# Kernel optimization log

Measured on AMD Instinct MI355X. Metric: run time of the kernel, lower is better.

The kernel has to match this reference:

```python
import jax, jax.numpy as jnp
import numpy as np

N = 1024    # num_points
HID = 1024  # Hamiltonian MLP hidden width


def setup_inputs() -> dict:
    key = jax.random.key(0)
    ks = jax.random.split(key, 6)
    def w(k, shape, fan_in):
        return jax.random.normal(k, shape, dtype=jnp.float32) / np.float32(np.sqrt(fan_in))
    return {
        "x": jax.random.normal(ks[0], (N,), dtype=jnp.float32),
        "q": jax.random.normal(ks[1], (N,), dtype=jnp.float32),
        "p": jax.random.normal(ks[2], (N,), dtype=jnp.float32),
        "W1": w(ks[3], (3 * N, HID), 3 * N),
        "b1": jnp.zeros((HID,), dtype=jnp.float32),
        "W2": w(ks[4], (HID, HID), HID),
        "b2": jnp.zeros((HID,), dtype=jnp.float32),
        "W3": w(ks[5], (HID, 1), HID),
        "b3": jnp.zeros((1,), dtype=jnp.float32),
    }


def _hamiltonian(z, W1, b1, W2, b2, W3, b3):
    # H: R^{3N} -> scalar (matches self.H(cat([x,q,p])).sum())
    h = jnp.tanh(z @ W1 + b1)
    h = jnp.tanh(h @ W2 + b2)
    return jnp.sum(h @ W3 + b3)


def reference(x, q, p, W1, b1, W2, b2, W3, b3):
    n = x.shape[0]

    def grads_qp(x_):
        # (dH/dq, dH/dp) as a function of x, with q,p closed over
        f = lambda q_, p_: _hamiltonian(jnp.concatenate([x_, q_, p_]), W1, b1, W2, b2, W3, b3)
        return jax.grad(f, argnums=(0, 1))(q, p)  # each [n]

    # Diagonal of cross-Hessian blocks via forward-over-reverse, batched over
    # all n basis directions at once (replaces the per-index autograd loop).
    eye = jnp.eye(n, dtype=x.dtype)

    def diag_entry(e_i, i):
        _, (dgq, dgp) = jax.jvp(grads_qp, (x,), (e_i,))
        return dgq[i], dgp[i]  # d2H/(dx_i dq_i), d2H/(dx_i dp_i)

    dH_dq_dx, dH_dp_dx = jax.vmap(diag_entry)(eye, jnp.arange(n))  # each [n]
    return dH_dp_dx, -dH_dq_dx
```

## Files before the change

### kernel.cpp

```cpp
#include <hip/hip_runtime.h>
#include <math.h>

typedef unsigned short u16;
typedef __bf16 bf16x8 __attribute__((ext_vector_type(8)));
typedef float f32x4 __attribute__((ext_vector_type(4)));

__device__ inline u16 bf16_rn(float x) {
    unsigned u = __float_as_uint(x);
    return (u16)((u + 0x7FFFu + ((u >> 16) & 1u)) >> 16);
}
__device__ inline uint2 pack4(u16 a, u16 b, u16 c, u16 d) {
    uint2 r;
    r.x = (unsigned)a | ((unsigned)b << 16);
    r.y = (unsigned)c | ((unsigned)d << 16);
    return r;
}
__device__ inline uint2 pack4f(float a, float b, float c, float d) {
    return pack4(bf16_rn(a), bf16_rn(b), bf16_rn(c), bf16_rn(d));
}
__device__ inline f32x4 mfma16(bf16x8 a, bf16x8 b, f32x4 c) {
    return __builtin_amdgcn_mfma_f32_16x16x32_bf16(a, b, c, 0, 0, 0);
}

__global__ __launch_bounds__(256) void k_pre(const float* __restrict__ x,
                                             const float* __restrict__ q,
                                             const float* __restrict__ p,
                                             const float* __restrict__ W1,
                                             u16* __restrict__ Ah,
                                             float* __restrict__ Upart,
                                             float* __restrict__ out,
                                             float* __restrict__ Vacc) {
    int b = blockIdx.x, t = threadIdx.x;
    if (b < 192) {
        int jc = b;
        int k = (jc & 3) * 256 + t;
        int j0 = (jc >> 2) * 64;
        __shared__ float zs[64];
        if (t < 64) {
            int j = j0 + t;
            zs[t] = (j < 1024) ? x[j] : (j < 2048 ? q[j - 1024] : p[j - 2048]);
        }
        __syncthreads();
        float acc = 0.f;
        if (j0 < 1024) {
#pragma unroll 8
            for (int j = 0; j < 64; ++j) {
                float v = W1[(j0 + j) * 1024 + k];
                Ah[(j0 + j) * 1024 + k] = bf16_rn(v);
                acc += zs[j] * v;
            }
        } else {
#pragma unroll 8
            for (int j = 0; j < 64; ++j) acc += zs[j] * W1[(j0 + j) * 1024 + k];
        }
        Upart[(jc >> 2) * 1024 + k] = acc;
    } else {
        int idx = ((b - 192) * 256 + t) * 4;
        if (idx < 2048) *(float4*)(out + idx) = make_float4(0.f, 0.f, 0.f, 0.f);
        else *(float4*)(Vacc + idx - 2048) = make_float4(0.f, 0.f, 0.f, 0.f);
    }
}

__global__ __launch_bounds__(256) void k_w2v(const float* __restrict__ W2,
                                             const float* __restrict__ b1,
                                             const float* __restrict__ Upart,
                                             float* __restrict__ H1g, float* __restrict__ D1g,
                                             u16* __restrict__ W2h,
                                             u16* __restrict__ WTh,
                                             float* __restrict__ Vacc) {
    __shared__ float T[64][65];
    __shared__ float hs[64], ds[64];
    __shared__ float red[4][64];
    int k0 = blockIdx.y * 64, m0 = blockIdx.x * 64;
    int t = threadIdx.x;
    {
        int lk = t & 63, g = t >> 6;
        float u = 0.f;
#pragma unroll
        for (int c = 0; c < 12; ++c) u += Upart[(g * 12 + c) * 1024 + k0 + lk];
        red[g][lk] = u;
    }
    __syncthreads();
    if (t < 64) {
        float u = red[0][t] + red[1][t] + red[2][t] + red[3][t];
        float h = tanhf(u + b1[k0 + t]);
        hs[t] = h;
        ds[t] = 1.f - h * h;
        if (m0 == 0) { H1g[k0 + t] = h; D1g[k0 + t] = 1.f - h * h; }
    }
    __syncthreads();
    int rr = t >> 4, cc = (t & 15) * 4;
    float4 vp = make_float4(0.f, 0.f, 0.f, 0.f);
#pragma unroll
    for (int j = 0; j < 4; ++j) {
        int r = rr + j * 16;
        float4 v = *(const float4*)(W2 + (k0 + r) * 1024 + m0 + cc);
        T[r][cc + 0] = v.x; T[r][cc + 1] = v.y; T[r][cc + 2] = v.z; T[r][cc + 3] = v.w;
        *(uint2*)&W2h[(k0 + r) * 1024 + m0 + cc] = pack4f(v.x, v.y, v.z, v.w);
        float hk = hs[r];
        vp.x += hk * v.x; vp.y += hk * v.y; vp.z += hk * v.z; vp.w += hk * v.w;
    }
    vp.x += __shfl_xor(vp.x, 16); vp.y += __shfl_xor(vp.y, 16);
    vp.z += __shfl_xor(vp.z, 16); vp.w += __shfl_xor(vp.w, 16);
    vp.x += __shfl_xor(vp.x, 32); vp.y += __shfl_xor(vp.y, 32);
    vp.z += __shfl_xor(vp.z, 32); vp.w += __shfl_xor(vp.w, 32);
    if (((t & 63) >> 4) == 0) {
        atomicAdd(&Vacc[m0 + cc + 0], vp.x);
        atomicAdd(&Vacc[m0 + cc + 1], vp.y);
        atomicAdd(&Vacc[m0 + cc + 2], vp.z);
        atomicAdd(&Vacc[m0 + cc + 3], vp.w);
    }
    __syncthreads();
#pragma unroll
    for (int j = 0; j < 4; ++j) {
        int mrow = rr + j * 16;
        float f0 = T[cc + 0][mrow] * ds[cc + 0];
        float f1 = T[cc + 1][mrow] * ds[cc + 1];
        float f2 = T[cc + 2][mrow] * ds[cc + 2];
        float f3 = T[cc + 3][mrow] * ds[cc + 3];
        *(uint2*)&WTh[(m0 + mrow) * 1024 + k0 + cc] = pack4f(f0, f1, f2, f3);
    }
}

#define LDK 68
__global__ __launch_bounds__(512) void k_gemm1(const u16* __restrict__ Ah,
                                               const u16* __restrict__ Bh,
                                               const float* __restrict__ Vacc,
                                               const float* __restrict__ b2,
                                               const float* __restrict__ W3,
                                               const float* __restrict__ W2,
                                               const float* __restrict__ H1,
                                               const float* __restrict__ D1,
                                               float* __restrict__ Avec,
                                               u16* __restrict__ Sh) {
    __shared__ u16 As[2][64 * LDK];
    __shared__ u16 Bs[2][64 * LDK];
    __shared__ float sv[1024];
    int tid = threadIdx.x;
    if (blockIdx.x == 16) {
        int kbase = blockIdx.y * 64;
#pragma unroll
        for (int j = 0; j < 2; ++j) {
            int m = tid + j * 512;
            float h = tanhf(Vacc[m] + b2[m]);
            sv[m] = (1.f - h * h) * W3[m];
        }
        __syncthreads();
        int g = tid >> 3, sub = tid & 7;
        int k = kbase + g;
        const float* wrow = W2 + k * 1024 + sub * 128;
        const float* svp = sv + sub * 128;
        float acc = 0.f;
#pragma unroll 8
        for (int j = 0; j < 128; ++j) acc += wrow[j] * svp[j];
        acc += __shfl_xor(acc, 1);
        acc += __shfl_xor(acc, 2);
        acc += __shfl_xor(acc, 4);
        if (sub == 0) Avec[k] = -2.f * H1[k] * D1[k] * acc;
        return;
    }
    int lane = tid & 63, wv = tid >> 6;
    int kh = wv >> 2, wy = (wv >> 1) & 1, wx = wv & 1;
    int i0 = blockIdx.y * 64, m0 = blockIdx.x * 64;
    int srow = tid >> 3, sseg = (tid & 7) * 8;
    int ldso = srow * LDK + sseg;
    const u16* ap = Ah + (i0 + srow) * 1024 + sseg;
    const u16* bp = Bh + (m0 + srow) * 1024 + sseg;
    int tx = lane & 15, qy = lane >> 4;
    int koff = kh * 32 + qy * 8;
    int raA[2], rbB[2];
    raA[0] = (wy * 32 + tx) * LDK + koff;
    raA[1] = raA[0] + 16 * LDK;
    rbB[0] = (wx * 32 + tx) * LDK + koff;
    rbB[1] = rbB[0] + 16 * LDK;
    f32x4 acc[2][2];
#pragma unroll
    for (int a = 0; a < 2; ++a)
#pragma unroll
        for (int b = 0; b < 2; ++b) acc[a][b] = (f32x4){0.f, 0.f, 0.f, 0.f};

    uint4 pa1 = *(const uint4*)(ap + 64);
    uint4 pc1 = *(const uint4*)(bp + 64);
    *(uint4*)&As[0][ldso] = *(const uint4*)(ap);
    *(uint4*)&Bs[0][ldso] = *(const uint4*)(bp);

    for (int k0 = 0; k0 < 1024; k0 += 64) {
        int buf = (k0 >> 6) & 1;
        int kn2 = (k0 + 128) & 1023;
        uint4 pa2 = *(const uint4*)(ap + kn2);
        uint4 pc2 = *(const uint4*)(bp + kn2);
        __syncthreads();
        bf16x8 aH0 = *(const bf16x8*)&As[buf][raA[0]];
        bf16x8 aH1 = *(const bf16x8*)&As[buf][raA[1]];
        bf16x8 bH0 = *(const bf16x8*)&Bs[buf][rbB[0]];
        bf16x8 bH1 = *(const bf16x8*)&Bs[buf][rbB[1]];
        acc[0][0] = mfma16(aH0, bH0, acc[0][0]);
        acc[0][1] = mfma16(aH0, bH1, acc[0][1]);
        acc[1][0] = mfma16(aH1, bH0, acc[1][0]);
        acc[1][1] = mfma16(aH1, bH1, acc[1][1]);
        int nb = buf ^ 1;
        *(uint4*)&As[nb][ldso] = pa1;
        *(uint4*)&Bs[nb][ldso] = pc1;
        pa1 = pa2; pc1 = pc2;
    }
    __syncthreads();
    f32x4* mrg = (f32x4*)&As[0][0];
    if (kh == 1) {
#pragma unroll
        for (int si = 0; si < 2; ++si)
#pragma unroll
            for (int sj = 0; sj < 2; ++sj)
                mrg[(((wy * 2 + wx) * 4 + si * 2 + sj) * 4 + qy) * 16 + tx] = acc[si][sj];
    }
    __syncthreads();
    if (kh == 0) {
#pragma unroll
        for (int si = 0; si < 2; ++si)
#pragma unroll
            for (int sj = 0; sj < 2; ++sj) {
                f32x4 o = mrg[(((wy * 2 + wx) * 4 + si * 2 + sj) * 4 + qy) * 16 + tx];
                acc[si][sj][0] += o[0]; acc[si][sj][1] += o[1];
                acc[si][sj][2] += o[2]; acc[si][sj][3] += o[3];
            }
#pragma unroll
        for (int sj = 0; sj < 2; ++sj) {
            int m = m0 + wx * 32 + sj * 16 + tx;
            float hv = tanhf(Vacc[m] + b2[m]);
            float d2 = 1.f - hv * hv;
            float cm = -2.f * hv * d2 * W3[m];
#pragma unroll
            for (int si = 0; si < 2; ++si) {
                int ib = i0 + wy * 32 + si * 16 + qy * 4;
#pragma unroll
                for (int r = 0; r < 4; ++r)
                    Sh[(ib + r) * 1024 + m] = bf16_rn(acc[si][sj][r] * cm);
            }
        }
    }
}

__global__ __launch_bounds__(512) void k_gemm2(const u16* __restrict__ Sh,
                                               const u16* __restrict__ W2h,
                                               const float* __restrict__ W1,
                                               const float* __restrict__ D1,
                                               const float* __restrict__ Avec,
                                               float* __restrict__ out) {
    __shared__ u16 As[2][64 * LDK];
    __shared__ u16 Bs[2][64 * LDK];
    int tid = threadIdx.x, lane = tid & 63, wv = tid >> 6;
    int kh = wv >> 2, wy = (wv >> 1) & 1, wx = wv & 1;
    int i0 = blockIdx.y * 64, k0g = blockIdx.x * 64;
    int srow = tid >> 3, sseg = (tid & 7) * 8;
    int ldso = srow * LDK + sseg;
    const u16* ap = Sh + (i0 + srow) * 1024 + sseg;
    const u16* bp = W2h + (k0g + srow) * 1024 + sseg;
    int tx = lane & 15, qy = lane >> 4;
    int koff = kh * 32 + qy * 8;
    int raA[2], rbB[2];
    raA[0] = (wy * 32 + tx) * LDK + koff;
    raA[1] = raA[0] + 16 * LDK;
    rbB[0] = (wx * 32 + tx) * LDK + koff;
    rbB[1] = rbB[0] + 16 * LDK;
    f32x4 acc[2][2];
#pragma unroll
    for (int a = 0; a < 2; ++a)
#pragma unroll
        for (int b = 0; b < 2; ++b) acc[a][b] = (f32x4){0.f, 0.f, 0.f, 0.f};

    uint4 pa1 = *(const uint4*)(ap + 64);
    uint4 pc1 = *(const uint4*)(bp + 64);
    *(uint4*)&As[0][ldso] = *(const uint4*)(ap);
    *(uint4*)&Bs[0][ldso] = *(const uint4*)(bp);

    for (int m0 = 0; m0 < 1024; m0 += 64) {
        int buf = (m0 >> 6) & 1;
        int mn2 = (m0 + 128) & 1023;
        uint4 pa2 = *(const uint4*)(ap + mn2);
        uint4 pc2 = *(const uint4*)(bp + mn2);
        __syncthreads();
        bf16x8 aH0 = *(const bf16x8*)&As[buf][raA[0]];
        bf16x8 aH1 = *(const bf16x8*)&As[buf][raA[1]];
        bf16x8 bH0 = *(const bf16x8*)&Bs[buf][rbB[0]];
        bf16x8 bH1 = *(const bf16x8*)&Bs[buf][rbB[1]];
        acc[0][0] = mfma16(aH0, bH0, acc[0][0]);
        acc[0][1] = mfma16(aH0, bH1, acc[0][1]);
        acc[1][0] = mfma16(aH1, bH0, acc[1][0]);
        acc[1][1] = mfma16(aH1, bH1, acc[1][1]);
        int nb = buf ^ 1;
        *(uint4*)&As[nb][ldso] = pa1;
        *(uint4*)&Bs[nb][ldso] = pc1;
        pa1 = pa2; pc1 = pc2;
    }
    __syncthreads();
    f32x4* mrg = (f32x4*)&As[0][0];
    if (kh == 1) {
#pragma unroll
        for (int si = 0; si < 2; ++si)
#pragma unroll
            for (int sj = 0; sj < 2; ++sj)
                mrg[(((wy * 2 + wx) * 4 + si * 2 + sj) * 4 + qy) * 16 + tx] = acc[si][sj];
    }
    __syncthreads();
    if (kh == 0) {
#pragma unroll
        for (int si = 0; si < 2; ++si)
#pragma unroll
            for (int sj = 0; sj < 2; ++sj) {
                f32x4 o = mrg[(((wy * 2 + wx) * 4 + si * 2 + sj) * 4 + qy) * 16 + tx];
                acc[si][sj][0] += o[0]; acc[si][sj][1] += o[1];
                acc[si][sj][2] += o[2]; acc[si][sj][3] += o[3];
            }
        int kk[2];
        float d1v[2], avv[2];
#pragma unroll
        for (int sj = 0; sj < 2; ++sj) {
            kk[sj] = k0g + wx * 32 + sj * 16 + tx;
            d1v[sj] = D1[kk[sj]];
            avv[sj] = Avec[kk[sj]];
        }
#pragma unroll
        for (int si = 0; si < 2; ++si) {
            int ib = i0 + wy * 32 + si * 16 + qy * 4;
#pragma unroll
            for (int r = 0; r < 4; ++r) {
                int i = ib + r;
                float pq = 0.f, pp = 0.f;
#pragma unroll
                for (int sj = 0; sj < 2; ++sj) {
                    int k = kk[sj];
                    float dr = avv[sj] * W1[i * 1024 + k] + d1v[sj] * acc[si][sj][r];
                    pq += W1[(1024 + i) * 1024 + k] * dr;
                    pp += W1[(2048 + i) * 1024 + k] * dr;
                }
                for (int o = 1; o < 16; o <<= 1) {
                    pq += __shfl_xor(pq, o);
                    pp += __shfl_xor(pp, o);
                }
                if (tx == 0) {
                    atomicAdd(&out[i], pp);
                    atomicAdd(&out[1024 + i], -pq);
                }
            }
        }
    }
}

extern "C" void kernel_launch(void* const* d_in, const int* in_sizes, int n_in,
                              void* d_out, int out_size, void* d_ws, size_t ws_size,
                              hipStream_t stream) {
    const float* x = (const float*)d_in[0];
    const float* q = (const float*)d_in[1];
    const float* p = (const float*)d_in[2];
    const float* W1 = (const float*)d_in[3];
    const float* b1 = (const float*)d_in[4];
    const float* W2 = (const float*)d_in[5];
    const float* b2 = (const float*)d_in[6];
    const float* W3 = (const float*)d_in[7];
    float* out = (float*)d_out;
    float* ws = (float*)d_ws;
    float* H1 = ws, *D1 = ws + 1024, *Avec = ws + 2048, *Vacc = ws + 3072;
    float* Upart = ws + 4096;
    u16* u0 = (u16*)(ws + 65536);
    u16* Ah = u0;
    u16* WTh = u0 + 1048576;
    u16* W2h = u0 + 2097152;
    u16* Sh = u0 + 3145728;

    k_pre<<<195, 256, 0, stream>>>(x, q, p, W1, Ah, Upart, out, Vacc);
    k_w2v<<<dim3(16, 16), 256, 0, stream>>>(W2, b1, Upart, H1, D1, W2h, WTh, Vacc);
    k_gemm1<<<dim3(17, 16), 512, 0, stream>>>(Ah, WTh, Vacc, b2, W3, W2, H1, D1, Avec, Sh);
    k_gemm2<<<dim3(16, 16), 512, 0, stream>>>(Sh, W2h, W1, D1, Avec, out);
}
```

Measured before the change: 119.2 us.

## Replace two chained GEMMs with one triple-accumulator GEMM over x,q,p W1 slices

Reformulates the Hessian-diagonal computation so that one GEMM, WT scaled by D1, multiplies all three W1 row blocks (x, q, p) against the same B tile. The result is reduced elementwise with the layer-2 coefficient, replacing the old gemm1 -> Sh -> gemm2 chain. The Avec term is moved into extra blocks that compute it and apply the W1 triple product directly with atomics. This removes the intermediate Sh round trip, the bf16 copy of W2 and one kernel launch. In exchange, the single GEMM reads three A tiles per step, uses more registers and shared memory, and converts all of W1 to bf16.

After: 164.8 us. 1.38x slower.

```diff
diff --git a/kernel.cpp b/kernel.cpp
--- a/kernel.cpp
+++ b/kernel.cpp
@@ -42,16 +42,11 @@
         }
         __syncthreads();
         float acc = 0.f;
-        if (j0 < 1024) {
 #pragma unroll 8
-            for (int j = 0; j < 64; ++j) {
-                float v = W1[(j0 + j) * 1024 + k];
-                Ah[(j0 + j) * 1024 + k] = bf16_rn(v);
-                acc += zs[j] * v;
-            }
-        } else {
-#pragma unroll 8
-            for (int j = 0; j < 64; ++j) acc += zs[j] * W1[(j0 + j) * 1024 + k];
+        for (int j = 0; j < 64; ++j) {
+            float v = W1[(j0 + j) * 1024 + k];
+            Ah[(j0 + j) * 1024 + k] = bf16_rn(v);
+            acc += zs[j] * v;
         }
         Upart[(jc >> 2) * 1024 + k] = acc;
     } else {
@@ -65,7 +60,6 @@
                                              const float* __restrict__ b1,
                                              const float* __restrict__ Upart,
                                              float* __restrict__ H1g, float* __restrict__ D1g,
-                                             u16* __restrict__ W2h,
                                              u16* __restrict__ WTh,
                                              float* __restrict__ Vacc) {
     __shared__ float T[64][65];
@@ -96,7 +90,6 @@
         int r = rr + j * 16;
         float4 v = *(const float4*)(W2 + (k0 + r) * 1024 + m0 + cc);
         T[r][cc + 0] = v.x; T[r][cc + 1] = v.y; T[r][cc + 2] = v.z; T[r][cc + 3] = v.w;
-        *(uint2*)&W2h[(k0 + r) * 1024 + m0 + cc] = pack4f(v.x, v.y, v.z, v.w);
         float hk = hs[r];
         vp.x += hk * v.x; vp.y += hk * v.y; vp.z += hk * v.z; vp.w += hk * v.w;
     }
@@ -123,22 +116,25 @@
 }
 
 #define LDK 68
-__global__ __launch_bounds__(512) void k_gemm1(const u16* __restrict__ Ah,
-                                               const u16* __restrict__ Bh,
-                                               const float* __restrict__ Vacc,
-                                               const float* __restrict__ b2,
-                                               const float* __restrict__ W3,
-                                               const float* __restrict__ W2,
-                                               const float* __restrict__ H1,
-                                               const float* __restrict__ D1,
-                                               float* __restrict__ Avec,
-                                               u16* __restrict__ Sh) {
-    __shared__ u16 As[2][64 * LDK];
-    __shared__ u16 Bs[2][64 * LDK];
-    __shared__ float sv[1024];
-    int tid = threadIdx.x;
-    if (blockIdx.x == 16) {
-        int kbase = blockIdx.y * 64;
+#define TILE_E (64 * LDK)
+#define SMEM_BYTES 69632
+__global__ __launch_bounds__(512) void k_big(const u16* __restrict__ Ah,
+                                             const u16* __restrict__ WTh,
+                                             const float* __restrict__ W1,
+                                             const float* __restrict__ W2,
+                                             const float* __restrict__ b2,
+                                             const float* __restrict__ W3,
+                                             const float* __restrict__ Vacc,
+                                             const float* __restrict__ H1,
+                                             const float* __restrict__ D1,
+                                             float* __restrict__ out) {
+    __shared__ __align__(16) char smem[SMEM_BYTES];
+    int tid = threadIdx.x, bid = blockIdx.x;
+
+    if (bid >= 256) {
+        float* sv = (float*)smem;
+        float* avL = (float*)(smem + 4096);
+        int kb = (bid - 256) * 16;
 #pragma unroll
         for (int j = 0; j < 2; ++j) {
             int m = tid + j * 512;
@@ -146,71 +142,121 @@
             sv[m] = (1.f - h * h) * W3[m];
         }
         __syncthreads();
-        int g = tid >> 3, sub = tid & 7;
-        int k = kbase + g;
-        const float* wrow = W2 + k * 1024 + sub * 128;
-        const float* svp = sv + sub * 128;
-        float acc = 0.f;
+        {
+            int row = tid >> 5, seg = tid & 31;
+            const float* wr = W2 + (kb + row) * 1024 + seg * 32;
+            const float* svp = sv + seg * 32;
+            float a = 0.f;
 #pragma unroll 8
-        for (int j = 0; j < 128; ++j) acc += wrow[j] * svp[j];
-        acc += __shfl_xor(acc, 1);
-        acc += __shfl_xor(acc, 2);
-        acc += __shfl_xor(acc, 4);
-        if (sub == 0) Avec[k] = -2.f * H1[k] * D1[k] * acc;
+            for (int j = 0; j < 32; ++j) a += wr[j] * svp[j];
+            a += __shfl_xor(a, 1); a += __shfl_xor(a, 2); a += __shfl_xor(a, 4);
+            a += __shfl_xor(a, 8); a += __shfl_xor(a, 16);
+            if (seg == 0) avL[row] = -2.f * H1[kb + row] * D1[kb + row] * a;
+        }
+        __syncthreads();
+        {
+            int kloc = tid & 15, ig = tid >> 4;
+            float av = avL[kloc];
+            int k = kb + kloc;
+            for (int it = 0; it < 32; ++it) {
+                int i = it * 32 + ig;
+                float wx = W1[i * 1024 + k];
+                float wq = W1[(1024 + i) * 1024 + k];
+                float wp = W1[(2048 + i) * 1024 + k];
+                float tv = av * wx;
+                float pq = tv * wq, pp = tv * wp;
+                pq += __shfl_xor(pq, 1); pp += __shfl_xor(pp, 1);
+                pq += __shfl_xor(pq, 2); pp += __shfl_xor(pp, 2);
+                pq += __shfl_xor(pq, 4); pp += __shfl_xor(pp, 4);
+                pq += __shfl_xor(pq, 8); pp += __shfl_xor(pp, 8);
+                if (kloc == 0) {
+                    atomicAdd(&out[i], pp);
+                    atomicAdd(&out[1024 + i], -pq);
+                }
+            }
+        }
         return;
     }
+
+    u16* Axs = (u16*)smem;
+    u16* Aqs = (u16*)(smem + 17408);
+    u16* Aps = (u16*)(smem + 34816);
+    u16* Bs  = (u16*)(smem + 52224);
     int lane = tid & 63, wv = tid >> 6;
     int kh = wv >> 2, wy = (wv >> 1) & 1, wx = wv & 1;
-    int i0 = blockIdx.y * 64, m0 = blockIdx.x * 64;
+    int i0 = (bid >> 4) * 64, m0 = (bid & 15) * 64;
     int srow = tid >> 3, sseg = (tid & 7) * 8;
     int ldso = srow * LDK + sseg;
-    const u16* ap = Ah + (i0 + srow) * 1024 + sseg;
-    const u16* bp = Bh + (m0 + srow) * 1024 + sseg;
+    const u16* apx = Ah + (i0 + srow) * 1024 + sseg;
+    const u16* apq = Ah + (1024 + i0 + srow) * 1024 + sseg;
+    const u16* app = Ah + (2048 + i0 + srow) * 1024 + sseg;
+    const u16* bp  = WTh + (m0 + srow) * 1024 + sseg;
     int tx = lane & 15, qy = lane >> 4;
     int koff = kh * 32 + qy * 8;
-    int raA[2], rbB[2];
-    raA[0] = (wy * 32 + tx) * LDK + koff;
-    raA[1] = raA[0] + 16 * LDK;
-    rbB[0] = (wx * 32 + tx) * LDK + koff;
-    rbB[1] = rbB[0] + 16 * LDK;
-    f32x4 acc[2][2];
+    int raA0 = (wy * 32 + tx) * LDK + koff, raA1 = raA0 + 16 * LDK;
+    int rbB0 = (wx * 32 + tx) * LDK + koff, rbB1 = rbB0 + 16 * LDK;
+    f32x4 accX[2][2], accQ[2][2], accP[2][2];
 #pragma unroll
     for (int a = 0; a < 2; ++a)
 #pragma unroll
-        for (int b = 0; b < 2; ++b) acc[a][b] = (f32x4){0.f, 0.f, 0.f, 0.f};
-
-    uint4 pa1 = *(const uint4*)(ap + 64);
-    uint4 pc1 = *(const uint4*)(bp + 64);
-    *(uint4*)&As[0][ldso] = *(const uint4*)(ap);
-    *(uint4*)&Bs[0][ldso] = *(const uint4*)(bp);
+        for (int b = 0; b < 2; ++b) {
+            accX[a][b] = (f32x4){0.f, 0.f, 0.f, 0.f};
+            accQ[a][b] = (f32x4){0.f, 0.f, 0.f, 0.f};
+            accP[a][b] = (f32x4){0.f, 0.f, 0.f, 0.f};
+        }
+
+    uint4 px1 = *(const uint4*)(apx + 64);
+    uint4 pq1 = *(const uint4*)(apq + 64);
+    uint4 pp1 = *(const uint4*)(app + 64);
+    uint4 pb1 = *(const uint4*)(bp + 64);
+    *(uint4*)&Axs[ldso] = *(const uint4*)(apx);
+    *(uint4*)&Aqs[ldso] = *(const uint4*)(apq);
+    *(uint4*)&Aps[ldso] = *(const uint4*)(app);
+    *(uint4*)&Bs[ldso]  = *(const uint4*)(bp);
 
     for (int k0 = 0; k0 < 1024; k0 += 64) {
-        int buf = (k0 >> 6) & 1;
+        int buf = ((k0 >> 6) & 1) * TILE_E;
         int kn2 = (k0 + 128) & 1023;
-        uint4 pa2 = *(const uint4*)(ap + kn2);
-        uint4 pc2 = *(const uint4*)(bp + kn2);
+        uint4 px2 = *(const uint4*)(apx + kn2);
+        uint4 pq2 = *(const uint4*)(apq + kn2);
+        uint4 pp2 = *(const uint4*)(app + kn2);
+        uint4 pb2 = *(const uint4*)(bp + kn2);
         __syncthreads();
-        bf16x8 aH0 = *(const bf16x8*)&As[buf][raA[0]];
-        bf16x8 aH1 = *(const bf16x8*)&As[buf][raA[1]];
-        bf16x8 bH0 = *(const bf16x8*)&Bs[buf][rbB[0]];
-        bf16x8 bH1 = *(const bf16x8*)&Bs[buf][rbB[1]];
-        acc[0][0] = mfma16(aH0, bH0, acc[0][0]);
-        acc[0][1] = mfma16(aH0, bH1, acc[0][1]);
-        acc[1][0] = mfma16(aH1, bH0, acc[1][0]);
-        acc[1][1] = mfma16(aH1, bH1, acc[1][1]);
-        int nb = buf ^ 1;
-        *(uint4*)&As[nb][ldso] = pa1;
-        *(uint4*)&Bs[nb][ldso] = pc1;
-        pa1 = pa2; pc1 = pc2;
-    }
-    __syncthreads();
-    f32x4* mrg = (f32x4*)&As[0][0];
+        bf16x8 bH0 = *(const bf16x8*)&Bs[buf + rbB0];
+        bf16x8 bH1 = *(const bf16x8*)&Bs[buf + rbB1];
+        bf16x8 aX0 = *(const bf16x8*)&Axs[buf + raA0];
+        bf16x8 aX1 = *(const bf16x8*)&Axs[buf + raA1];
+        bf16x8 aQ0 = *(const bf16x8*)&Aqs[buf + raA0];
+        bf16x8 aQ1 = *(const bf16x8*)&Aqs[buf + raA1];
+        bf16x8 aP0 = *(const bf16x8*)&Aps[buf + raA0];
+        bf16x8 aP1 = *(const bf16x8*)&Aps[buf + raA1];
+        accX[0][0] = mfma16(aX0, bH0, accX[0][0]);
+        accX[0][1] = mfma16(aX0, bH1, accX[0][1]);
+        accX[1][0] = mfma16(aX1, bH0, accX[1][0]);
+        accX[1][1] = mfma16(aX1, bH1, accX[1][1]);
+        accQ[0][0] = mfma16(aQ0, bH0, accQ[0][0]);
+        accQ[0][1] = mfma16(aQ0, bH1, accQ[0][1]);
+        accQ[1][0] = mfma16(aQ1, bH0, accQ[1][0]);
+        accQ[1][1] = mfma16(aQ1, bH1, accQ[1][1]);
+        accP[0][0] = mfma16(aP0, bH0, accP[0][0]);
+        accP[0][1] = mfma16(aP0, bH1, accP[0][1]);
+        accP[1][0] = mfma16(aP1, bH0, accP[1][0]);
+        accP[1][1] = mfma16(aP1, bH1, accP[1][1]);
+        int nb = buf ^ TILE_E;
+        *(uint4*)&Axs[nb + ldso] = px1;
+        *(uint4*)&Aqs[nb + ldso] = pq1;
+        *(uint4*)&Aps[nb + ldso] = pp1;
+        *(uint4*)&Bs[nb + ldso]  = pb1;
+        px1 = px2; pq1 = pq2; pp1 = pp2; pb1 = pb2;
+    }
+    f32x4* mrg = (f32x4*)smem;
+#define MRG_IDX(si, sj) ((((wy * 2 + wx) * 4 + (si) * 2 + (sj)) * 4 + qy) * 16 + tx)
+    __syncthreads();
     if (kh == 1) {
 #pragma unroll
         for (int si = 0; si < 2; ++si)
 #pragma unroll
-            for (int sj = 0; sj < 2; ++sj)
-                mrg[(((wy * 2 + wx) * 4 + si * 2 + sj) * 4 + qy) * 16 + tx] = acc[si][sj];
+            for (int sj = 0; sj < 2; ++sj) mrg[MRG_IDX(si, sj)] = accX[si][sj];
     }
     __syncthreads();
     if (kh == 0) {
@@ -218,105 +264,53 @@
         for (int si = 0; si < 2; ++si)
 #pragma unroll
             for (int sj = 0; sj < 2; ++sj) {
-                f32x4 o = mrg[(((wy * 2 + wx) * 4 + si * 2 + sj) * 4 + qy) * 16 + tx];
-                acc[si][sj][0] += o[0]; acc[si][sj][1] += o[1];
-                acc[si][sj][2] += o[2]; acc[si][sj][3] += o[3];
-            }
+                f32x4 o = mrg[MRG_IDX(si, sj)];
+                accX[si][sj][0] += o[0]; accX[si][sj][1] += o[1];
+                accX[si][sj][2] += o[2]; accX[si][sj][3] += o[3];
+            }
+    }
+    __syncthreads();
+    if (kh == 1) {
+#pragma unroll
+        for (int si = 0; si < 2; ++si)
+#pragma unroll
+            for (int sj = 0; sj < 2; ++sj) mrg[MRG_IDX(si, sj)] = accQ[si][sj];
+    }
+    __syncthreads();
+    if (kh == 0) {
+#pragma unroll
+        for (int si = 0; si < 2; ++si)
+#pragma unroll
+            for (int sj = 0; sj < 2; ++sj) {
+                f32x4 o = mrg[MRG_IDX(si, sj)];
+                accQ[si][sj][0] += o[0]; accQ[si][sj][1] += o[1];
+                accQ[si][sj][2] += o[2]; accQ[si][sj][3] += o[3];
+            }
+    }
+    __syncthreads();
+    if (kh == 1) {
+#pragma unroll
+        for (int si = 0; si < 2; ++si)
+#pragma unroll
+            for (int sj = 0; sj < 2; ++sj) mrg[MRG_IDX(si, sj)] = accP[si][sj];
+    }
+    __syncthreads();
+    if (kh == 0) {
+#pragma unroll
+        for (int si = 0; si < 2; ++si)
+#pragma unroll
+            for (int sj = 0; sj < 2; ++sj) {
+                f32x4 o = mrg[MRG_IDX(si, sj)];
+                accP[si][sj][0] += o[0]; accP[si][sj][1] += o[1];
+                accP[si][sj][2] += o[2]; accP[si][sj][3] += o[3];
+            }
+        float cm[2];
 #pragma unroll
         for (int sj = 0; sj < 2; ++sj) {
             int m = m0 + wx * 32 + sj * 16 + tx;
             float hv = tanhf(Vacc[m] + b2[m]);
             float d2 = 1.f - hv * hv;
-            float cm = -2.f * hv * d2 * W3[m];
-#pragma unroll
-            for (int si = 0; si < 2; ++si) {
-                int ib = i0 + wy * 32 + si * 16 + qy * 4;
-#pragma unroll
-                for (int r = 0; r < 4; ++r)
-                    Sh[(ib + r) * 1024 + m] = bf16_rn(acc[si][sj][r] * cm);
-            }
-        }
-    }
-}
-
-__global__ __launch_bounds__(512) void k_gemm2(const u16* __restrict__ Sh,
-                                               const u16* __restrict__ W2h,
-                                               const float* __restrict__ W1,
-                                               const float* __restrict__ D1,
-                                               const float* __restrict__ Avec,
-                                               float* __restrict__ out) {
-    __shared__ u16 As[2][64 * LDK];
-    __shared__ u16 Bs[2][64 * LDK];
-    int tid = threadIdx.x, lane = tid & 63, wv = tid >> 6;
-    int kh = wv >> 2, wy = (wv >> 1) & 1, wx = wv & 1;
-    int i0 = blockIdx.y * 64, k0g = blockIdx.x * 64;
-    int srow = tid >> 3, sseg = (tid & 7) * 8;
-    int ldso = srow * LDK + sseg;
-    const u16* ap = Sh + (i0 + srow) * 1024 + sseg;
-    const u16* bp = W2h + (k0g + srow) * 1024 + sseg;
-    int tx = lane & 15, qy = lane >> 4;
-    int koff = kh * 32 + qy * 8;
-    int raA[2], rbB[2];
-    raA[0] = (wy * 32 + tx) * LDK + koff;
-    raA[1] = raA[0] + 16 * LDK;
-    rbB[0] = (wx * 32 + tx) * LDK + koff;
-    rbB[1] = rbB[0] + 16 * LDK;
-    f32x4 acc[2][2];
-#pragma unroll
-    for (int a = 0; a < 2; ++a)
-#pragma unroll
-        for (int b = 0; b < 2; ++b) acc[a][b] = (f32x4){0.f, 0.f, 0.f, 0.f};
-
-    uint4 pa1 = *(const uint4*)(ap + 64);
-    uint4 pc1 = *(const uint4*)(bp + 64);
-    *(uint4*)&As[0][ldso] = *(const uint4*)(ap);
-    *(uint4*)&Bs[0][ldso] = *(const uint4*)(bp);
-
-    for (int m0 = 0; m0 < 1024; m0 += 64) {
-        int buf = (m0 >> 6) & 1;
-        int mn2 = (m0 + 128) & 1023;
-        uint4 pa2 = *(const uint4*)(ap + mn2);
-        uint4 pc2 = *(const uint4*)(bp + mn2);
-        __syncthreads();
-        bf16x8 aH0 = *(const bf16x8*)&As[buf][raA[0]];
-        bf16x8 aH1 = *(const bf16x8*)&As[buf][raA[1]];
-        bf16x8 bH0 = *(const bf16x8*)&Bs[buf][rbB[0]];
-        bf16x8 bH1 = *(const bf16x8*)&Bs[buf][rbB[1]];
-        acc[0][0] = mfma16(aH0, bH0, acc[0][0]);
-        acc[0][1] = mfma16(aH0, bH1, acc[0][1]);
-        acc[1][0] = mfma16(aH1, bH0, acc[1][0]);
-        acc[1][1] = mfma16(aH1, bH1, acc[1][1]);
-        int nb = buf ^ 1;
-        *(uint4*)&As[nb][ldso] = pa1;
-        *(uint4*)&Bs[nb][ldso] = pc1;
-        pa1 = pa2; pc1 = pc2;
-    }
-    __syncthreads();
-    f32x4* mrg = (f32x4*)&As[0][0];
-    if (kh == 1) {
-#pragma unroll
-        for (int si = 0; si < 2; ++si)
-#pragma unroll
-            for (int sj = 0; sj < 2; ++sj)
-                mrg[(((wy * 2 + wx) * 4 + si * 2 + sj) * 4 + qy) * 16 + tx] = acc[si][sj];
-    }
-    __syncthreads();
-    if (kh == 0) {
-#pragma unroll
-        for (int si = 0; si < 2; ++si)
-#pragma unroll
-            for (int sj = 0; sj < 2; ++sj) {
-                f32x4 o = mrg[(((wy * 2 + wx) * 4 + si * 2 + sj) * 4 + qy) * 16 + tx];
-                acc[si][sj][0] += o[0]; acc[si][sj][1] += o[1];
-                acc[si][sj][2] += o[2]; acc[si][sj][3] += o[3];
-            }
-        int kk[2];
-        float d1v[2], avv[2];
-#pragma unroll
-        for (int sj = 0; sj < 2; ++sj) {
-            kk[sj] = k0g + wx * 32 + sj * 16 + tx;
-            d1v[sj] = D1[kk[sj]];
-            avv[sj] = Avec[kk[sj]];
+            cm[sj] = -2.f * hv * d2 * W3[m];
         }
 #pragma unroll
         for (int si = 0; si < 2; ++si) {
@@ -327,10 +321,9 @@
                 float pq = 0.f, pp = 0.f;
 #pragma unroll
                 for (int sj = 0; sj < 2; ++sj) {
-                    int k = kk[sj];
-                    float dr = avv[sj] * W1[i * 1024 + k] + d1v[sj] * acc[si][sj][r];
-                    pq += W1[(1024 + i) * 1024 + k] * dr;
-                    pp += W1[(2048 + i) * 1024 + k] * dr;
+                    float mx = accX[si][sj][r];
+                    pq += cm[sj] * mx * accQ[si][sj][r];
+                    pp += cm[sj] * mx * accP[si][sj][r];
                 }
                 for (int o = 1; o < 16; o <<= 1) {
                     pq += __shfl_xor(pq, o);
@@ -358,16 +351,13 @@
     const float* W3 = (const float*)d_in[7];
     float* out = (float*)d_out;
     float* ws = (float*)d_ws;
-    float* H1 = ws, *D1 = ws + 1024, *Avec = ws + 2048, *Vacc = ws + 3072;
+    float* H1 = ws, *D1 = ws + 1024, *Vacc = ws + 3072;
     float* Upart = ws + 4096;
     u16* u0 = (u16*)(ws + 65536);
     u16* Ah = u0;
-    u16* WTh = u0 + 1048576;
-    u16* W2h = u0 + 2097152;
-    u16* Sh = u0 + 3145728;
+    u16* WTh = u0 + 3145728;
 
     k_pre<<<195, 256, 0, stream>>>(x, q, p, W1, Ah, Upart, out, Vacc);
-    k_w2v<<<dim3(16, 16), 256, 0, stream>>>(W2, b1, Upart, H1, D1, W2h, WTh, Vacc);
-    k_gemm1<<<dim3(17, 16), 512, 0, stream>>>(Ah, WTh, Vacc, b2, W3, W2, H1, D1, Avec, Sh);
-    k_gemm2<<<dim3(16, 16), 512, 0, stream>>>(Sh, W2h, W1, D1, Avec, out);
-}
+    k_w2v<<<dim3(16, 16), 256, 0, stream>>>(W2, b1, Upart, H1, D1, WTh, Vacc);
+    k_big<<<320, 512, 0, stream>>>(Ah, WTh, W1, W2, b2, W3, Vacc, H1, D1, out);
+}
```
